# Performance work log

Measured on AMD Instinct MI355X. Metric: run time of the kernel, lower is better.

The kernel has to match this reference:

```python
import jax, jax.numpy as jnp
import numpy as np

K_NEIGHBORS = 5  # sklearn KNNImputer default n_neighbors, weights='uniform'


def _impute_feature(Xz, present):
    # Xz: [N, T1] feature values with 0 at missing entries; present: [N, T1] bool.
    # sklearn nan_euclidean distance: sqrt(T1/cnt * sum_valid (x_i - y_i)^2),
    # valid dims = both present; cnt==0 -> excluded (treated as inf here).
    T1 = Xz.shape[1]
    pf = present.astype(Xz.dtype)
    sq = Xz * Xz
    d2 = sq @ pf.T + pf @ sq.T - 2.0 * (Xz @ Xz.T)  # [N, N]
    cnt = pf @ pf.T
    d2 = jnp.maximum(d2, 0.0) * (jnp.asarray(T1, Xz.dtype) / jnp.maximum(cnt, 1.0))
    dist = jnp.sqrt(d2)
    dist = jnp.where(cnt > 0, dist, jnp.inf)
    # distances only pick neighbors (piecewise-constant wrt values)
    dist = jax.lax.stop_gradient(dist)

    def impute_col(xcol, prescol):
        # donors must have a value in this column and a finite distance
        d = jnp.where(prescol[None, :], dist, jnp.inf)  # [N, N]
        negv, idx = jax.lax.top_k(-d, K_NEIGHBORS)       # k smallest distances
        sel_ok = jnp.isfinite(negv)                      # [N, K]
        vals = xcol[idx]                                 # [N, K] donor values
        cntk = sel_ok.sum(-1)
        mean_k = (vals * sel_ok).sum(-1) / jnp.maximum(cntk, 1)
        # fallback: observed column mean when no valid donor (sklearn behavior)
        colmean = (xcol * prescol).sum() / jnp.maximum(prescol.sum(), 1)
        imput = jnp.where(cntk > 0, mean_k, colmean)
        return jnp.where(prescol, xcol, imput)  # [N]

    # vmap over the T1 columns -> [T1, N]
    return jax.vmap(impute_col, in_axes=(1, 1))(Xz, present)


def reference(x_all, mask):
    # x_all: [T1, N, D_in] stacked node features (steps + output graph)
    # mask:  [T1, N] int, 1 = missing (original code: last channel of x)
    T1, N, D_in = x_all.shape
    C = D_in - 1  # output_node_dim
    present = (mask == 0).T  # [N, T1]
    outs = []
    for c in range(C):
        X = x_all[..., c].T                      # [N, T1]
        Xz = jnp.where(present, X, 0.0)
        steps = _impute_feature(Xz, present)     # [T1, N]
        outs.append(steps[-1])                   # last step = output graph
    return jnp.stack(outs, axis=-1)              # [N, C] -> h_v


def setup_inputs() -> dict:
    key = jax.random.key(0)
    k1, k2 = jax.random.split(key)
    x_all = jax.random.normal(k1, (17, 2048, 9), dtype=jnp.float32)
    mask = jax.random.randint(k2, (17, 2048), 0, 2, dtype=jnp.int32)
    return {"x_all": x_all, "mask": mask}
```

## Files before the change

kernel.cpp:

```cpp
#include <hip/hip_runtime.h>
#include <math.h>

#define T1 17
#define NN 2048
#define DIN 9
#define CC 8
#define KK 5
#define NSTR 5
#define NDCAP (NSTR * 256)
#define NQCAP 1280
#define LPAD (NDCAP + 8)
#define NU (NDCAP / 64)

#define XD_BYTES (T1 * NN * CC * 4)

__global__ __launch_bounds__(1024) void prep_kernel(
    const float* __restrict__ x_all, const int* __restrict__ mask,
    unsigned* __restrict__ pm, int* __restrict__ dlist,
    unsigned* __restrict__ pmd, int* __restrict__ qlist,
    float* __restrict__ colmean, int* __restrict__ cnts,
    float* __restrict__ out) {
  __shared__ unsigned long long dbal[32];
  __shared__ int dpre[33], qpre[33];
  __shared__ float wsum[16][CC];
  const int tid = threadIdx.x;
  const int lane = tid & 63, w = tid >> 6;

  unsigned m0 = 0, m1 = 0;
#pragma unroll
  for (int t = 0; t < T1; ++t) {
    m0 |= (mask[t * NN + tid] == 0 ? 1u : 0u) << t;
    m1 |= (mask[t * NN + tid + 1024] == 0 ? 1u : 0u) << t;
  }
  pm[tid] = m0;
  pm[tid + 1024] = m1;
  const bool v0 = (m0 >> 16) & 1u, v1 = (m1 >> 16) & 1u;
  const unsigned long long b0 = __ballot(v0), b1 = __ballot(v1);
  if (lane == 0) { dbal[w] = b0; dbal[16 + w] = b1; }

  float s[CC];
#pragma unroll
  for (int c = 0; c < CC; ++c) s[c] = 0.f;
  if (v0) {
    const float* row = x_all + ((size_t)16 * NN + tid) * DIN;
#pragma unroll
    for (int c = 0; c < CC; ++c) { const float v = row[c]; s[c] = v; out[tid * CC + c] = v; }
  }
  if (v1) {
    const float* row = x_all + ((size_t)16 * NN + tid + 1024) * DIN;
#pragma unroll
    for (int c = 0; c < CC; ++c) { const float v = row[c]; s[c] += v; out[(tid + 1024) * CC + c] = v; }
  }
#pragma unroll
  for (int off = 32; off > 0; off >>= 1) {
#pragma unroll
    for (int c = 0; c < CC; ++c) s[c] += __shfl_down(s[c], off);
  }
  if (lane == 0) {
#pragma unroll
    for (int c = 0; c < CC; ++c) wsum[w][c] = s[c];
  }
  __syncthreads();

  if (tid == 0) {
    int a = 0, b = 0;
    for (int g = 0; g < 32; ++g) {
      dpre[g] = a;
      qpre[g] = b;
      const int p = (int)__popcll(dbal[g]);
      a += p;
      b += 64 - p;
    }
    dpre[32] = a;
    qpre[32] = b;
    cnts[0] = a;
    cnts[1] = b;
  }
  __syncthreads();

  const unsigned long long ltm = (1ull << lane) - 1ull;
  if (v0) {
    const int p = dpre[w] + (int)__popcll(b0 & ltm);
    dlist[p] = tid; pmd[p] = m0;
  } else {
    const int p = qpre[w] + (int)__popcll((~b0) & ltm);
    qlist[p] = tid;
  }
  if (v1) {
    const int p = dpre[16 + w] + (int)__popcll(b1 & ltm);
    dlist[p] = tid + 1024; pmd[p] = m1;
  } else {
    const int p = qpre[16 + w] + (int)__popcll((~b1) & ltm);
    qlist[p] = tid + 1024;
  }

  if (tid < CC) {
    float tot = 0.f;
#pragma unroll
    for (int ww = 0; ww < 16; ++ww) tot += wsum[ww][tid];
    colmean[tid] = tot / fmaxf((float)dpre[32], 1.f);
  }
}

__global__ void transpose_kernel(const float* __restrict__ x_all,
                                 const int* __restrict__ dlist,
                                 const int* __restrict__ cnts,
                                 float* __restrict__ xd) {
  const int u = blockIdx.x * 256 + threadIdx.x;
  if (u >= T1 * NN * CC) return;
  const int t = u / (NN * CC);
  const int rem = u % (NN * CC);
  const int dn = rem >> 3;
  const int c = rem & 7;
  if (dn < cnts[0]) xd[u] = x_all[((size_t)t * NN + dlist[dn]) * DIN + c];
}

__global__ __launch_bounds__(512, 3) void knn_main(
    const float* __restrict__ x_all, const float* __restrict__ xd,
    const unsigned* __restrict__ pm, const unsigned* __restrict__ pmd,
    const int* __restrict__ qlist, const int* __restrict__ cnts,
    const float* __restrict__ colmean, float* __restrict__ out) {
  __shared__ float sdist[CC][LPAD];
  __shared__ float qlds[T1][CC];
  __shared__ float rcp17[32];
  const int nq = cnts[1];
  const int bid = blockIdx.x;
  if (bid >= nq) return;
  const int i = qlist[bid];
  const int ndon = cnts[0];
  const unsigned mi = pm[i];
  const int tid = threadIdx.x;

  if (tid < 32) rcp17[tid] = 17.f / (float)tid;
  if (tid < 16 * CC)
    qlds[tid >> 3][tid & 7] = x_all[((size_t)(tid >> 3) * NN + i) * DIN + (tid & 7)];
  if (tid >= 16 * CC && tid < 17 * CC) qlds[16][tid & 7] = 0.f;
  __syncthreads();

  const int qd = tid & 1;
  const int c0 = qd * 4;
  const int dg = tid >> 1;
  const int lane = tid & 63;
  const int w = tid >> 6;

  float a0[NSTR], a1[NSTR], a2[NSTR], a3[NSTR];
  unsigned ms[NSTR];
#pragma unroll
  for (int s = 0; s < NSTR; ++s) {
    const int dn = dg + 256 * s;
    ms[s] = (dn < ndon) ? (mi & pmd[dn]) : 0u;
    a0[s] = a1[s] = a2[s] = a3[s] = 0.f;
  }
  const int nstr_act = (ndon + 255) >> 8;

  unsigned tm = mi & 0xFFFFu;
  while (tm) {
    const int t0 = __ffs(tm) - 1;
    tm &= tm - 1u;
    const int t1 = tm ? (__ffs(tm) - 1) : 16;
    tm = tm ? (tm & (tm - 1u)) : 0u;
    const float4 qv0 = *(const float4*)&qlds[t0][c0];
    const float4 qv1 = *(const float4*)&qlds[t1][c0];
#pragma unroll
    for (int s = 0; s < NSTR; ++s) {
      if (s < nstr_act) {
        const int dn = dg + 256 * s;
        const float4 dv0 = *(const float4*)&xd[((size_t)t0 * NN + dn) * CC + c0];
        const float4 dv1 = *(const float4*)&xd[((size_t)t1 * NN + dn) * CC + c0];
        const float fl0 = (float)((ms[s] >> t0) & 1u);
        const float fl1 = (float)((ms[s] >> t1) & 1u);
        float e;
        e = qv0.x - dv0.x; a0[s] = fmaf(e * e, fl0, a0[s]);
        e = qv0.y - dv0.y; a1[s] = fmaf(e * e, fl0, a1[s]);
        e = qv0.z - dv0.z; a2[s] = fmaf(e * e, fl0, a2[s]);
        e = qv0.w - dv0.w; a3[s] = fmaf(e * e, fl0, a3[s]);
        e = qv1.x - dv1.x; a0[s] = fmaf(e * e, fl1, a0[s]);
        e = qv1.y - dv1.y; a1[s] = fmaf(e * e, fl1, a1[s]);
        e = qv1.z - dv1.z; a2[s] = fmaf(e * e, fl1, a2[s]);
        e = qv1.w - dv1.w; a3[s] = fmaf(e * e, fl1, a3[s]);
      }
    }
  }

#pragma unroll
  for (int s = 0; s < NSTR; ++s) {
    const int dn = dg + 256 * s;
    const int cnt = __popc(ms[s]);
    const float sc = rcp17[cnt & 31];
    const bool ok = cnt > 0;
    sdist[c0 + 0][dn] = ok ? sqrtf(a0[s] * sc) : INFINITY;
    sdist[c0 + 1][dn] = ok ? sqrtf(a1[s] * sc) : INFINITY;
    sdist[c0 + 2][dn] = ok ? sqrtf(a2[s] * sc) : INFINITY;
    sdist[c0 + 3][dn] = ok ? sqrtf(a3[s] * sc) : INFINITY;
  }
  __syncthreads();

  float dvr[NU];
#pragma unroll
  for (int u = 0; u < NU; ++u) dvr[u] = sdist[w][u * 64 + lane];

  float sum = 0.f;
  int cn = 0;
#pragma unroll
  for (int k = 0; k < KK; ++k) {
    float g = dvr[0];
#pragma unroll
    for (int u = 1; u < NU; ++u) g = fminf(g, dvr[u]);
#pragma unroll
    for (int off = 32; off > 0; off >>= 1) g = fminf(g, __shfl_xor(g, off));
    if (g < INFINITY) {
      int jloc = 0x7FFFFFFF;
#pragma unroll
      for (int u = NU - 1; u >= 0; --u)
        if (dvr[u] == g) jloc = u * 64 + lane;
      int jg = jloc;
#pragma unroll
      for (int off = 32; off > 0; off >>= 1) jg = min(jg, __shfl_xor(jg, off));
      const int jgs = __builtin_amdgcn_readfirstlane(jg);
      const int tu = jgs >> 6, tl = jgs & 63;
#pragma unroll
      for (int u = 0; u < NU; ++u)
        if (u == tu) dvr[u] = (lane == tl) ? INFINITY : dvr[u];
      sum += xd[((size_t)16 * NN + jgs) * CC + w];
      ++cn;
    }
  }
  if (lane == 0) out[i * CC + w] = (cn > 0) ? sum / (float)cn : colmean[w];
}

extern "C" void kernel_launch(void* const* d_in, const int* in_sizes, int n_in,
                              void* d_out, int out_size, void* d_ws, size_t ws_size,
                              hipStream_t stream) {
  const float* x_all = (const float*)d_in[0];
  const int* mask = (const int*)d_in[1];
  float* out = (float*)d_out;

  char* ws = (char*)d_ws;
  float* xd = (float*)ws;
  unsigned* pm = (unsigned*)(ws + XD_BYTES);
  int* dlist = (int*)(ws + XD_BYTES + NN * 4);
  unsigned* pmd = (unsigned*)(ws + XD_BYTES + NN * 8);
  int* qlist = (int*)(ws + XD_BYTES + NN * 12);
  float* colmean = (float*)(ws + XD_BYTES + NN * 16);
  int* cnts = (int*)(ws + XD_BYTES + NN * 16 + CC * 4);

  prep_kernel<<<1, 1024, 0, stream>>>(x_all, mask, pm, dlist, pmd, qlist, colmean, cnts, out);
  transpose_kernel<<<(T1 * NN * CC + 255) / 256, 256, 0, stream>>>(x_all, dlist, cnts, xd);
  knn_main<<<NQCAP, 512, 0, stream>>>(x_all, xd, pm, pmd, qlist, cnts, colmean, out);
}
```

Before: 45.38 us.

## Split single-block prep into parallel mask pass and compaction kernel; skip empty donor strides

Result: slower. 46.30 us (+2.0%).

```diff
diff --git a/kernel.cpp b/kernel.cpp
--- a/kernel.cpp
+++ b/kernel.cpp
@@ -11,63 +11,65 @@
 #define NQCAP 1280
 #define LPAD (NDCAP + 8)
 #define NU (NDCAP / 64)
+#define PLANE (NN * CC)
 
 #define XD_BYTES (T1 * NN * CC * 4)
 
-__global__ __launch_bounds__(1024) void prep_kernel(
+__global__ __launch_bounds__(128) void prep_a(
     const float* __restrict__ x_all, const int* __restrict__ mask,
-    unsigned* __restrict__ pm, int* __restrict__ dlist,
+    unsigned* __restrict__ pm, unsigned long long* __restrict__ wsbal,
+    float* __restrict__ wscol, float* __restrict__ out) {
+  const int row = blockIdx.x * 128 + threadIdx.x;
+  const int lane = threadIdx.x & 63;
+  const int g = row >> 6;
+  unsigned m = 0;
+#pragma unroll
+  for (int t = 0; t < T1; ++t)
+    m |= (mask[t * NN + row] == 0 ? 1u : 0u) << t;
+  pm[row] = m;
+  const bool v = (m >> 16) & 1u;
+  const unsigned long long bal = __ballot(v);
+
+  float s[CC];
+#pragma unroll
+  for (int c = 0; c < CC; ++c) s[c] = 0.f;
+  if (v) {
+    const float* r = x_all + ((size_t)16 * NN + row) * DIN;
+#pragma unroll
+    for (int c = 0; c < CC; ++c) {
+      const float vv = r[c];
+      s[c] = vv;
+      out[row * CC + c] = vv;
+    }
+  }
+#pragma unroll
+  for (int off = 32; off > 0; off >>= 1) {
+#pragma unroll
+    for (int c = 0; c < CC; ++c) s[c] += __shfl_down(s[c], off);
+  }
+  if (lane == 0) {
+    wsbal[g] = bal;
+#pragma unroll
+    for (int c = 0; c < CC; ++c) wscol[g * CC + c] = s[c];
+  }
+}
+
+__global__ __launch_bounds__(1024) void prep_b(
+    const unsigned* __restrict__ pm, const unsigned long long* __restrict__ wsbal,
+    const float* __restrict__ wscol, int* __restrict__ dlist,
     unsigned* __restrict__ pmd, int* __restrict__ qlist,
-    float* __restrict__ colmean, int* __restrict__ cnts,
-    float* __restrict__ out) {
-  __shared__ unsigned long long dbal[32];
+    float* __restrict__ colmean, int* __restrict__ cnts) {
   __shared__ int dpre[33], qpre[33];
-  __shared__ float wsum[16][CC];
+  __shared__ unsigned long long sbal[32];
   const int tid = threadIdx.x;
-  const int lane = tid & 63, w = tid >> 6;
-
-  unsigned m0 = 0, m1 = 0;
-#pragma unroll
-  for (int t = 0; t < T1; ++t) {
-    m0 |= (mask[t * NN + tid] == 0 ? 1u : 0u) << t;
-    m1 |= (mask[t * NN + tid + 1024] == 0 ? 1u : 0u) << t;
-  }
-  pm[tid] = m0;
-  pm[tid + 1024] = m1;
-  const bool v0 = (m0 >> 16) & 1u, v1 = (m1 >> 16) & 1u;
-  const unsigned long long b0 = __ballot(v0), b1 = __ballot(v1);
-  if (lane == 0) { dbal[w] = b0; dbal[16 + w] = b1; }
-
-  float s[CC];
-#pragma unroll
-  for (int c = 0; c < CC; ++c) s[c] = 0.f;
-  if (v0) {
-    const float* row = x_all + ((size_t)16 * NN + tid) * DIN;
-#pragma unroll
-    for (int c = 0; c < CC; ++c) { const float v = row[c]; s[c] = v; out[tid * CC + c] = v; }
-  }
-  if (v1) {
-    const float* row = x_all + ((size_t)16 * NN + tid + 1024) * DIN;
-#pragma unroll
-    for (int c = 0; c < CC; ++c) { const float v = row[c]; s[c] += v; out[(tid + 1024) * CC + c] = v; }
-  }
-#pragma unroll
-  for (int off = 32; off > 0; off >>= 1) {
-#pragma unroll
-    for (int c = 0; c < CC; ++c) s[c] += __shfl_down(s[c], off);
-  }
-  if (lane == 0) {
-#pragma unroll
-    for (int c = 0; c < CC; ++c) wsum[w][c] = s[c];
-  }
-  __syncthreads();
-
+  if (tid < 32) sbal[tid] = wsbal[tid];
+  __syncthreads();
   if (tid == 0) {
     int a = 0, b = 0;
     for (int g = 0; g < 32; ++g) {
       dpre[g] = a;
       qpre[g] = b;
-      const int p = (int)__popcll(dbal[g]);
+      const int p = (int)__popcll(sbal[g]);
       a += p;
       b += 64 - p;
     }
@@ -77,27 +79,26 @@
     cnts[1] = b;
   }
   __syncthreads();
-
-  const unsigned long long ltm = (1ull << lane) - 1ull;
-  if (v0) {
-    const int p = dpre[w] + (int)__popcll(b0 & ltm);
-    dlist[p] = tid; pmd[p] = m0;
-  } else {
-    const int p = qpre[w] + (int)__popcll((~b0) & ltm);
-    qlist[p] = tid;
-  }
-  if (v1) {
-    const int p = dpre[16 + w] + (int)__popcll(b1 & ltm);
-    dlist[p] = tid + 1024; pmd[p] = m1;
-  } else {
-    const int p = qpre[16 + w] + (int)__popcll((~b1) & ltm);
-    qlist[p] = tid + 1024;
-  }
-
+#pragma unroll
+  for (int h = 0; h < 2; ++h) {
+    const int row = tid + h * 1024;
+    const unsigned m = pm[row];
+    const int g = row >> 6, l = row & 63;
+    const unsigned long long bal = sbal[g];
+    const unsigned long long ltm = (1ull << l) - 1ull;
+    if ((m >> 16) & 1u) {
+      const int p = dpre[g] + (int)__popcll(bal & ltm);
+      dlist[p] = row;
+      pmd[p] = m;
+    } else {
+      const int p = qpre[g] + (int)__popcll((~bal) & ltm);
+      qlist[p] = row;
+    }
+  }
   if (tid < CC) {
     float tot = 0.f;
 #pragma unroll
-    for (int ww = 0; ww < 16; ++ww) tot += wsum[ww][tid];
+    for (int g = 0; g < 32; ++g) tot += wscol[g * CC + tid];
     colmean[tid] = tot / fmaxf((float)dpre[32], 1.f);
   }
 }
@@ -128,7 +129,7 @@
   if (bid >= nq) return;
   const int i = qlist[bid];
   const int ndon = cnts[0];
-  const unsigned mi = pm[i];
+  const unsigned mi = (unsigned)__builtin_amdgcn_readfirstlane((int)pm[i]);
   const int tid = threadIdx.x;
 
   if (tid < 32) rcp17[tid] = 17.f / (float)tid;
@@ -145,28 +146,30 @@
 
   float a0[NSTR], a1[NSTR], a2[NSTR], a3[NSTR];
   unsigned ms[NSTR];
+  int eoff[NSTR];
 #pragma unroll
   for (int s = 0; s < NSTR; ++s) {
     const int dn = dg + 256 * s;
     ms[s] = (dn < ndon) ? (mi & pmd[dn]) : 0u;
+    eoff[s] = dn * CC + c0;
     a0[s] = a1[s] = a2[s] = a3[s] = 0.f;
   }
-  const int nstr_act = (ndon + 255) >> 8;
 
   unsigned tm = mi & 0xFFFFu;
   while (tm) {
     const int t0 = __ffs(tm) - 1;
     tm &= tm - 1u;
-    const int t1 = tm ? (__ffs(tm) - 1) : 16;
-    tm = tm ? (tm & (tm - 1u)) : 0u;
+    int t1 = 16;
+    if (tm) { t1 = __ffs(tm) - 1; tm &= tm - 1u; }
+    const float* __restrict__ p0 = xd + (size_t)t0 * PLANE;
+    const float* __restrict__ p1 = xd + (size_t)t1 * PLANE;
     const float4 qv0 = *(const float4*)&qlds[t0][c0];
     const float4 qv1 = *(const float4*)&qlds[t1][c0];
 #pragma unroll
     for (int s = 0; s < NSTR; ++s) {
-      if (s < nstr_act) {
-        const int dn = dg + 256 * s;
-        const float4 dv0 = *(const float4*)&xd[((size_t)t0 * NN + dn) * CC + c0];
-        const float4 dv1 = *(const float4*)&xd[((size_t)t1 * NN + dn) * CC + c0];
+      if (ms[s]) {
+        const float4 dv0 = *(const float4*)(p0 + eoff[s]);
+        const float4 dv1 = *(const float4*)(p1 + eoff[s]);
         const float fl0 = (float)((ms[s] >> t0) & 1u);
         const float fl1 = (float)((ms[s] >> t1) & 1u);
         float e;
@@ -243,8 +246,11 @@
   int* qlist = (int*)(ws + XD_BYTES + NN * 12);
   float* colmean = (float*)(ws + XD_BYTES + NN * 16);
   int* cnts = (int*)(ws + XD_BYTES + NN * 16 + CC * 4);
-
-  prep_kernel<<<1, 1024, 0, stream>>>(x_all, mask, pm, dlist, pmd, qlist, colmean, cnts, out);
+  unsigned long long* wsbal = (unsigned long long*)(ws + XD_BYTES + NN * 16 + CC * 4 + 64);
+  float* wscol = (float*)(ws + XD_BYTES + NN * 16 + CC * 4 + 64 + 32 * 8);
+
+  prep_a<<<16, 128, 0, stream>>>(x_all, mask, pm, wsbal, wscol, out);
+  prep_b<<<1, 1024, 0, stream>>>(pm, wsbal, wscol, dlist, pmd, qlist, colmean, cnts);
   transpose_kernel<<<(T1 * NN * CC + 255) / 256, 256, 0, stream>>>(x_all, dlist, cnts, xd);
   knn_main<<<NQCAP, 512, 0, stream>>>(x_all, xd, pm, pmd, qlist, cnts, colmean, out);
 }
```
